# Kernel tuning notes

Measured on AMD Instinct MI355X. Metric: run time of the kernel, lower is better.

The kernel has to match this reference:

```python
import jax, jax.numpy as jnp
import numpy as np


def setup_inputs() -> dict:
    key = jax.random.key(0)
    ks = jax.random.split(key, 8)
    bs, slen, d = 16, 2048, 1024
    scale = 1.0 / np.sqrt(d)
    return {
        "query": jax.random.normal(ks[0], (bs, d), jnp.float32),
        "states": jax.random.normal(ks[1], (bs, slen, d), jnp.float32),
        "Wq": jax.random.normal(ks[2], (d, d), jnp.float32) * scale,
        "bq": jax.random.normal(ks[3], (d,), jnp.float32) * 0.01,
        "Wk": jax.random.normal(ks[4], (d, d), jnp.float32) * scale,
        "bk": jax.random.normal(ks[5], (d,), jnp.float32) * 0.01,
        "We": jax.random.normal(ks[6], (2 * d,), jnp.float32) * scale,
        "be": jax.random.normal(ks[7], (1,), jnp.float32) * 0.01,
    }


def reference(query, states, Wq, bq, Wk, bk, We, be):
    d = Wq.shape[1]
    # q: (bs, d); k: (bs, slen, d)
    q = jax.nn.relu(query @ Wq + bq)
    k = jax.nn.relu(jnp.einsum("bsv,vd->bsd", states, Wk) + bk)
    # tanh(cat(q, k)) @ We == tanh(q) @ We[:d] + tanh(k) @ We[d:]
    # (avoids materializing the repeated/concatenated (bs, slen, 2d) tensor)
    We_q, We_k = We[:d], We[d:]
    energy = (jnp.tanh(q) @ We_q)[:, None] + jnp.einsum("bsd,d->bs", jnp.tanh(k), We_k) + be[0]
    attn_weights = jax.nn.softmax(energy, axis=1)  # (bs, slen)
    attn = jnp.einsum("bs,bsd->bd", attn_weights, states)  # weighted sum of values
    return attn_weights, attn
```

## Files before the change

### kernel.cpp

```cpp
#include <hip/hip_runtime.h>
#include <hip/hip_bf16.h>

#define D 1024
#define SLEN 2048
#define BS 16
#define MROWS (BS*SLEN)
#define CROWS 32
#define NCHUNK (MROWS/CROWS)
#define CPB (SLEN/CROWS)

typedef __attribute__((ext_vector_type(8))) short short8;
typedef __attribute__((ext_vector_type(4))) float f32x4;

__device__ __forceinline__ short f2bf(float f) {
  __hip_bfloat16 h = __float2bfloat16(f);
  return __builtin_bit_cast(short, h);
}

__device__ __forceinline__ float4 ntload4(const float* p) {
  f32x4 v = __builtin_nontemporal_load((const f32x4*)p);
  float4 r; r.x = v.x; r.y = v.y; r.z = v.z; r.w = v.w; return r;
}

__global__ __launch_bounds__(256) void wk_prep(const float* __restrict__ Wk,
                                               short* __restrict__ WkT) {
  const int g = blockIdx.x;
  const int t = threadIdx.x;
#pragma unroll
  for (int it = 0; it < 4; ++it) {
    const int n = it*256 + t;
    short8 p;
#pragma unroll
    for (int j = 0; j < 8; ++j)
      p[j] = f2bf(Wk[(size_t)(g*8 + j)*D + n]);
    *(short8*)(WkT + ((size_t)g*D + n)*8) = p;
  }
}

__global__ __launch_bounds__(512, 4) void energy_gemm(
    const float* __restrict__ states, const short* __restrict__ WkT,
    const float* __restrict__ bk, const float* __restrict__ We,
    float* __restrict__ eraw, float* __restrict__ pattn,
    float* __restrict__ cmax, float* __restrict__ csum)
{
  __shared__ short Al[CROWS * 129 * 8];
  __shared__ float red2[CROWS * 8];
  __shared__ float pfin[CROWS];

  const int tid  = threadIdx.x;
  const int w    = tid >> 6;
  const int lane = tid & 63;
  const int quad = lane >> 4;
  const int l16  = lane & 15;
  const int g    = blockIdx.x;
  const int m0   = g * CROWS;

  {
    const int row = tid >> 4;
    const int u0  = tid & 15;
    const float* Ag = states + (size_t)(m0 + row)*D;
#pragma unroll
    for (int i = 0; i < 8; ++i) {
      const int u = u0 + i*16;
      float4 x0 = ntload4(Ag + u*8);
      float4 x1 = ntload4(Ag + u*8 + 4);
      short8 p;
      p[0]=f2bf(x0.x); p[1]=f2bf(x0.y); p[2]=f2bf(x0.z); p[3]=f2bf(x0.w);
      p[4]=f2bf(x1.x); p[5]=f2bf(x1.y); p[6]=f2bf(x1.z); p[7]=f2bf(x1.w);
      *(short8*)(Al + ((size_t)row*129 + u)*8) = p;
    }
  }
  __syncthreads();

  f32x4 acc[2][2][4];
#pragma unroll
  for (int nc = 0; nc < 2; ++nc)
#pragma unroll
    for (int mi = 0; mi < 2; ++mi)
#pragma unroll
      for (int ni = 0; ni < 4; ++ni)
        acc[nc][mi][ni] = (f32x4){0.f, 0.f, 0.f, 0.f};

  const short* bbase = WkT + ((size_t)quad*D + w*128 + l16)*8;
  const short* abase = Al + ((size_t)l16*129 + quad)*8;

#pragma unroll 2
  for (int ks = 0; ks < 32; ++ks) {
    short8 fa[2], fbx[4];
#pragma unroll
    for (int mi = 0; mi < 2; ++mi)
      fa[mi] = *(const short8*)(abase + mi*16512 + ks*32);
    const short* bp = bbase + (size_t)ks*32768;
#pragma unroll
    for (int nc = 0; nc < 2; ++nc) {
#pragma unroll
      for (int ni = 0; ni < 4; ++ni)
        fbx[ni] = *(const short8*)(bp + nc*512 + ni*128);
#pragma unroll
      for (int mi = 0; mi < 2; ++mi)
#pragma unroll
        for (int ni = 0; ni < 4; ++ni)
          acc[nc][mi][ni] = __builtin_amdgcn_mfma_f32_16x16x32_bf16(
              fa[mi], fbx[ni], acc[nc][mi][ni], 0, 0, 0);
    }
  }

  float esum[8];
#pragma unroll
  for (int q = 0; q < 8; ++q) esum[q] = 0.f;
#pragma unroll
  for (int nc = 0; nc < 2; ++nc)
#pragma unroll
    for (int ni = 0; ni < 4; ++ni) {
      const int n = w*128 + nc*64 + ni*16 + l16;
      const float bkv = bk[n];
      const float wev = We[D + n];
#pragma unroll
      for (int mi = 0; mi < 2; ++mi)
#pragma unroll
        for (int r = 0; r < 4; ++r) {
          float x = acc[nc][mi][ni][r] + bkv;
          x = fmaxf(x, 0.f);
          float ex = __expf(2.f * x);
          float th = 1.f - 2.f/(ex + 1.f);
          esum[mi*4 + r] += th * wev;
        }
    }
#pragma unroll
  for (int dd = 1; dd < 16; dd <<= 1)
#pragma unroll
    for (int q = 0; q < 8; ++q)
      esum[q] += __shfl_xor(esum[q], dd, 64);

  if (l16 == 0) {
#pragma unroll
    for (int mi = 0; mi < 2; ++mi)
#pragma unroll
      for (int r = 0; r < 4; ++r)
        red2[(mi*16 + quad*4 + r)*8 + w] = esum[mi*4 + r];
  }
  __syncthreads();

  if (tid < CROWS) {
    float e = 0.f;
#pragma unroll
    for (int wi = 0; wi < 8; ++wi) e += red2[tid*8 + wi];
    eraw[m0 + tid] = e;
    float mm = e;
#pragma unroll
    for (int dd = 1; dd < 32; dd <<= 1) mm = fmaxf(mm, __shfl_xor(mm, dd, 64));
    const float pv = __expf(e - mm);
    float ss = pv;
#pragma unroll
    for (int dd = 1; dd < 32; dd <<= 1) ss += __shfl_xor(ss, dd, 64);
    pfin[tid] = pv;
    if (tid == 0) { cmax[g] = mm; csum[g] = ss; }
  }
  __syncthreads();

  {
    const int u    = tid >> 2;
    const int joff = (tid & 3) * 2;
    const short* ap = Al + (size_t)u*8 + joff;
    float a0 = 0.f, a1 = 0.f;
#pragma unroll 16
    for (int row = 0; row < CROWS; ++row) {
      const unsigned int bits = *(const unsigned int*)(ap + (size_t)row*1032);
      const float pv = pfin[row];
      const float lo = __builtin_bit_cast(float, bits << 16);
      const float hi = __builtin_bit_cast(float, bits & 0xffff0000u);
      a0 = fmaf(pv, lo, a0);
      a1 = fmaf(pv, hi, a1);
    }
    float2 o; o.x = a0; o.y = a1;
    *(float2*)(pattn + (size_t)g*D + 2*tid) = o;
  }
}

__global__ __launch_bounds__(256) void attn_finalize(
    const float* __restrict__ eraw, const float* __restrict__ pattn,
    const float* __restrict__ cmax, const float* __restrict__ csum,
    float* __restrict__ wts, float* __restrict__ attn)
{
  const int b = blockIdx.x;
  const int t = threadIdx.x;
  __shared__ float scl[CPB];
  __shared__ float stats[2];

  if (t < CPB) {
    const float m = cmax[b*CPB + t];
    float mm = m;
#pragma unroll
    for (int dd = 1; dd < 64; dd <<= 1) mm = fmaxf(mm, __shfl_xor(mm, dd, 64));
    const float e = __expf(m - mm);
    scl[t] = e;
    float s = e * csum[b*CPB + t];
#pragma unroll
    for (int dd = 1; dd < 64; dd <<= 1) s += __shfl_xor(s, dd, 64);
    if (t == 0) { stats[0] = mm; stats[1] = 1.f / s; }
  }
  __syncthreads();
  const float m_b = stats[0];
  const float inv = stats[1];

#pragma unroll
  for (int j = 0; j < 8; ++j) {
    const int s = j*256 + t;
    wts[(size_t)b*SLEN + s] = __expf(eraw[(size_t)b*SLEN + s] - m_b) * inv;
  }

  float acc[4] = {0.f, 0.f, 0.f, 0.f};
#pragma unroll
  for (int c = 0; c < CPB; ++c) {
    const float sc = scl[c];
    const float* pp = pattn + ((size_t)(b*CPB + c))*D + t;
#pragma unroll
    for (int j = 0; j < 4; ++j)
      acc[j] = fmaf(sc, pp[j*256], acc[j]);
  }
#pragma unroll
  for (int j = 0; j < 4; ++j)
    attn[(size_t)b*D + j*256 + t] = acc[j] * inv;
}

extern "C" void kernel_launch(void* const* d_in, const int* in_sizes, int n_in,
                              void* d_out, int out_size, void* d_ws, size_t ws_size,
                              hipStream_t stream) {
  const float* states = (const float*)d_in[1];
  const float* Wk     = (const float*)d_in[4];
  const float* bk     = (const float*)d_in[5];
  const float* We     = (const float*)d_in[6];
  float* out = (float*)d_out;

  char* ws = (char*)d_ws;
  short* WkT   = (short*)ws;  ws += (size_t)D*D*sizeof(short);
  float* eraw  = (float*)ws;  ws += (size_t)MROWS*sizeof(float);
  float* pattn = (float*)ws;  ws += (size_t)NCHUNK*D*sizeof(float);
  float* cmaxp = (float*)ws;  ws += (size_t)NCHUNK*sizeof(float);
  float* csump = (float*)ws;

  (void)in_sizes; (void)n_in; (void)out_size; (void)ws_size;

  wk_prep<<<128, 256, 0, stream>>>(Wk, WkT);
  energy_gemm<<<NCHUNK, 512, 0, stream>>>(states, WkT, bk, We, eraw, pattn, cmaxp, csump);
  attn_finalize<<<BS, 256, 0, stream>>>(eraw, pattn, cmaxp, csump, out, out + MROWS);
}
```

Baseline: 287.2 us.

## Double rows per block to 64 and use 16 waves sharing each Wk tile

Each energy_gemm block now processes 64 state rows with 1024 threads, and each of 16 waves covers 64 output columns across 4 row tiles instead of 128 columns across 2. Every bf16 Wk fragment read from global memory now feeds twice as many MFMAs, halving Wk traffic per row. The reductions, chunk softmax statistics and finalize shuffle widths are adjusted for the larger chunk. The LDS tile roughly doubles to about 132KB, which likely limits each CU to one block, so the staging phase and the MFMA phase no longer overlap across blocks.

Result: faster. 267.5 us (-6.9%).

```diff
diff --git a/kernel.cpp b/kernel.cpp
--- a/kernel.cpp
+++ b/kernel.cpp
@@ -5,7 +5,7 @@
 #define SLEN 2048
 #define BS 16
 #define MROWS (BS*SLEN)
-#define CROWS 32
+#define CROWS 64
 #define NCHUNK (MROWS/CROWS)
 #define CPB (SLEN/CROWS)
 
@@ -37,14 +37,14 @@
   }
 }
 
-__global__ __launch_bounds__(512, 4) void energy_gemm(
+__global__ __launch_bounds__(1024, 4) void energy_gemm(
     const float* __restrict__ states, const short* __restrict__ WkT,
     const float* __restrict__ bk, const float* __restrict__ We,
     float* __restrict__ eraw, float* __restrict__ pattn,
     float* __restrict__ cmax, float* __restrict__ csum)
 {
   __shared__ short Al[CROWS * 129 * 8];
-  __shared__ float red2[CROWS * 8];
+  __shared__ float red2[CROWS * 16];
   __shared__ float pfin[CROWS];
 
   const int tid  = threadIdx.x;
@@ -58,107 +58,110 @@
   {
     const int row = tid >> 4;
     const int u0  = tid & 15;
-    const float* Ag = states + (size_t)(m0 + row)*D;
-#pragma unroll
-    for (int i = 0; i < 8; ++i) {
-      const int u = u0 + i*16;
-      float4 x0 = ntload4(Ag + u*8);
-      float4 x1 = ntload4(Ag + u*8 + 4);
-      short8 p;
-      p[0]=f2bf(x0.x); p[1]=f2bf(x0.y); p[2]=f2bf(x0.z); p[3]=f2bf(x0.w);
-      p[4]=f2bf(x1.x); p[5]=f2bf(x1.y); p[6]=f2bf(x1.z); p[7]=f2bf(x1.w);
-      *(short8*)(Al + ((size_t)row*129 + u)*8) = p;
+#pragma unroll
+    for (int half = 0; half < 2; ++half) {
+      const float* Ag = states + (size_t)(m0 + row)*D;
+      float4 xs[8];
+#pragma unroll
+      for (int i = 0; i < 4; ++i) {
+        const int u = u0 + (half*4 + i)*16;
+        xs[2*i]   = ntload4(Ag + u*8);
+        xs[2*i+1] = ntload4(Ag + u*8 + 4);
+      }
+#pragma unroll
+      for (int i = 0; i < 4; ++i) {
+        const int u = u0 + (half*4 + i)*16;
+        short8 p;
+        p[0]=f2bf(xs[2*i].x);   p[1]=f2bf(xs[2*i].y);
+        p[2]=f2bf(xs[2*i].z);   p[3]=f2bf(xs[2*i].w);
+        p[4]=f2bf(xs[2*i+1].x); p[5]=f2bf(xs[2*i+1].y);
+        p[6]=f2bf(xs[2*i+1].z); p[7]=f2bf(xs[2*i+1].w);
+        *(short8*)(Al + ((size_t)row*129 + u)*8) = p;
+      }
     }
   }
   __syncthreads();
 
-  f32x4 acc[2][2][4];
-#pragma unroll
-  for (int nc = 0; nc < 2; ++nc)
-#pragma unroll
-    for (int mi = 0; mi < 2; ++mi)
-#pragma unroll
-      for (int ni = 0; ni < 4; ++ni)
-        acc[nc][mi][ni] = (f32x4){0.f, 0.f, 0.f, 0.f};
-
-  const short* bbase = WkT + ((size_t)quad*D + w*128 + l16)*8;
+  f32x4 acc[4][4];
+#pragma unroll
+  for (int mi = 0; mi < 4; ++mi)
+#pragma unroll
+    for (int ni = 0; ni < 4; ++ni)
+      acc[mi][ni] = (f32x4){0.f, 0.f, 0.f, 0.f};
+
+  const short* bbase = WkT + ((size_t)quad*D + w*64 + l16)*8;
   const short* abase = Al + ((size_t)l16*129 + quad)*8;
 
 #pragma unroll 2
   for (int ks = 0; ks < 32; ++ks) {
-    short8 fa[2], fbx[4];
-#pragma unroll
-    for (int mi = 0; mi < 2; ++mi)
+    short8 fa[4], fbx[4];
+#pragma unroll
+    for (int mi = 0; mi < 4; ++mi)
       fa[mi] = *(const short8*)(abase + mi*16512 + ks*32);
     const short* bp = bbase + (size_t)ks*32768;
 #pragma unroll
-    for (int nc = 0; nc < 2; ++nc) {
+    for (int ni = 0; ni < 4; ++ni)
+      fbx[ni] = *(const short8*)(bp + ni*128);
+#pragma unroll
+    for (int mi = 0; mi < 4; ++mi)
 #pragma unroll
       for (int ni = 0; ni < 4; ++ni)
-        fbx[ni] = *(const short8*)(bp + nc*512 + ni*128);
-#pragma unroll
-      for (int mi = 0; mi < 2; ++mi)
-#pragma unroll
-        for (int ni = 0; ni < 4; ++ni)
-          acc[nc][mi][ni] = __builtin_amdgcn_mfma_f32_16x16x32_bf16(
-              fa[mi], fbx[ni], acc[nc][mi][ni], 0, 0, 0);
-    }
-  }
-
-  float esum[8];
-#pragma unroll
-  for (int q = 0; q < 8; ++q) esum[q] = 0.f;
-#pragma unroll
-  for (int nc = 0; nc < 2; ++nc)
-#pragma unroll
-    for (int ni = 0; ni < 4; ++ni) {
-      const int n = w*128 + nc*64 + ni*16 + l16;
-      const float bkv = bk[n];
-      const float wev = We[D + n];
-#pragma unroll
-      for (int mi = 0; mi < 2; ++mi)
-#pragma unroll
-        for (int r = 0; r < 4; ++r) {
-          float x = acc[nc][mi][ni][r] + bkv;
-          x = fmaxf(x, 0.f);
-          float ex = __expf(2.f * x);
-          float th = 1.f - 2.f/(ex + 1.f);
-          esum[mi*4 + r] += th * wev;
-        }
-    }
+        acc[mi][ni] = __builtin_amdgcn_mfma_f32_16x16x32_bf16(
+            fa[mi], fbx[ni], acc[mi][ni], 0, 0, 0);
+  }
+
+  float esum[16];
+#pragma unroll
+  for (int q = 0; q < 16; ++q) esum[q] = 0.f;
+#pragma unroll
+  for (int ni = 0; ni < 4; ++ni) {
+    const int n = w*64 + ni*16 + l16;
+    const float bkv = bk[n];
+    const float wev = We[D + n];
+#pragma unroll
+    for (int mi = 0; mi < 4; ++mi)
+#pragma unroll
+      for (int r = 0; r < 4; ++r) {
+        float x = acc[mi][ni][r] + bkv;
+        x = fmaxf(x, 0.f);
+        float ex = __expf(2.f * x);
+        float th = 1.f - 2.f/(ex + 1.f);
+        esum[mi*4 + r] += th * wev;
+      }
+  }
 #pragma unroll
   for (int dd = 1; dd < 16; dd <<= 1)
 #pragma unroll
-    for (int q = 0; q < 8; ++q)
+    for (int q = 0; q < 16; ++q)
       esum[q] += __shfl_xor(esum[q], dd, 64);
 
   if (l16 == 0) {
 #pragma unroll
-    for (int mi = 0; mi < 2; ++mi)
+    for (int mi = 0; mi < 4; ++mi)
 #pragma unroll
       for (int r = 0; r < 4; ++r)
-        red2[(mi*16 + quad*4 + r)*8 + w] = esum[mi*4 + r];
+        red2[(mi*16 + quad*4 + r)*16 + w] = esum[mi*4 + r];
   }
   __syncthreads();
 
   if (tid < CROWS) {
     float e = 0.f;
 #pragma unroll
-    for (int wi = 0; wi < 8; ++wi) e += red2[tid*8 + wi];
+    for (int wi = 0; wi < 16; ++wi) e += red2[tid*16 + wi];
     eraw[m0 + tid] = e;
     float mm = e;
 #pragma unroll
-    for (int dd = 1; dd < 32; dd <<= 1) mm = fmaxf(mm, __shfl_xor(mm, dd, 64));
+    for (int dd = 1; dd < 64; dd <<= 1) mm = fmaxf(mm, __shfl_xor(mm, dd, 64));
     const float pv = __expf(e - mm);
     float ss = pv;
 #pragma unroll
-    for (int dd = 1; dd < 32; dd <<= 1) ss += __shfl_xor(ss, dd, 64);
+    for (int dd = 1; dd < 64; dd <<= 1) ss += __shfl_xor(ss, dd, 64);
     pfin[tid] = pv;
     if (tid == 0) { cmax[g] = mm; csum[g] = ss; }
   }
   __syncthreads();
 
-  {
+  if (tid < 512) {
     const int u    = tid >> 2;
     const int joff = (tid & 3) * 2;
     const short* ap = Al + (size_t)u*8 + joff;
@@ -191,12 +194,12 @@
     const float m = cmax[b*CPB + t];
     float mm = m;
 #pragma unroll
-    for (int dd = 1; dd < 64; dd <<= 1) mm = fmaxf(mm, __shfl_xor(mm, dd, 64));
+    for (int dd = 1; dd < CPB; dd <<= 1) mm = fmaxf(mm, __shfl_xor(mm, dd, 64));
     const float e = __expf(m - mm);
     scl[t] = e;
     float s = e * csum[b*CPB + t];
 #pragma unroll
-    for (int dd = 1; dd < 64; dd <<= 1) s += __shfl_xor(s, dd, 64);
+    for (int dd = 1; dd < CPB; dd <<= 1) s += __shfl_xor(s, dd, 64);
     if (t == 0) { stats[0] = mm; stats[1] = 1.f / s; }
   }
   __syncthreads();
@@ -242,6 +245,6 @@
   (void)in_sizes; (void)n_in; (void)out_size; (void)ws_size;
 
   wk_prep<<<128, 256, 0, stream>>>(Wk, WkT);
-  energy_gemm<<<NCHUNK, 512, 0, stream>>>(states, WkT, bk, We, eraw, pattn, cmaxp, csump);
+  energy_gemm<<<NCHUNK, 1024, 0, stream>>>(states, WkT, bk, We, eraw, pattn, cmaxp, csump);
   attn_finalize<<<BS, 256, 0, stream>>>(eraw, pattn, cmaxp, csump, out, out + MROWS);
 }
```
